# Kernel tuning notes

Measured on AMD Instinct MI355X. Metric: run time of the kernel, lower is better.

## Reference

```python
import jax, jax.numpy as jnp
import numpy as np

NUM_RELATIONS = 2
NUM_NODES = 100000


def rgcn_conv(x, edge_index, edge_type, weight, root, bias):
    """PyG RGCNConv with default aggr='mean':
    out[i] = bias + x[i] @ root + sum_r mean_{j in N_r(i)} (x[j] @ W_r)
    x: [N, Cin], edge_index: [2, E], weight: [R, Cin, Cout], root: [Cin, Cout]."""
    src, dst = edge_index[0], edge_index[1]
    x_src = x[src]                      # [E, Cin] gather
    out = x @ root + bias               # [N, Cout]
    for r in range(NUM_RELATIONS):      # small fixed loop over relations
        mask = (edge_type == r).astype(x.dtype)          # [E]
        msg = (x_src @ weight[r]) * mask[:, None]        # [E, Cout]
        agg = jax.ops.segment_sum(msg, dst, num_segments=NUM_NODES)
        deg = jax.ops.segment_sum(mask, dst, num_segments=NUM_NODES)
        out = out + agg / jnp.maximum(deg, 1.0)[:, None]
    return out


def setup_inputs() -> dict:
    key = jax.random.key(0)
    ks = jax.random.split(key, 16)
    Cin, Chid, Cout = 128, 256, 128
    E = 400000
    inp = {
        "x0": jax.random.normal(ks[0], (50000, 128), jnp.float32),
        "x1": jax.random.normal(ks[1], (50000, 64), jnp.float32),
        "edge_index": jax.random.randint(ks[2], (2, E), 0, NUM_NODES),
        "edge_type": jax.random.randint(ks[3], (E,), 0, NUM_RELATIONS),
        "dec_index": jax.random.randint(ks[4], (2, 100000), 0, NUM_NODES),
        # per-node-type input projections (Linear as x @ W + b)
        "lin0_w": jax.random.normal(ks[5], (128, Cin), jnp.float32) * 0.05,
        "lin0_b": jnp.zeros((Cin,), jnp.float32),
        "lin1_w": jax.random.normal(ks[6], (64, Cin), jnp.float32) * 0.05,
        "lin1_b": jnp.zeros((Cin,), jnp.float32),
        # RGCN layer 1
        "conv1_w": jax.random.normal(ks[7], (NUM_RELATIONS, Cin, Chid), jnp.float32) * 0.05,
        "conv1_root": jax.random.normal(ks[8], (Cin, Chid), jnp.float32) * 0.05,
        "conv1_b": jnp.zeros((Chid,), jnp.float32),
        # RGCN layer 2
        "conv2_w": jax.random.normal(ks[9], (NUM_RELATIONS, Chid, Cout), jnp.float32) * 0.05,
        "conv2_root": jax.random.normal(ks[10], (Chid, Cout), jnp.float32) * 0.05,
        "conv2_b": jnp.zeros((Cout,), jnp.float32),
        # decode head: Linear(2*Cout -> 1) + sigmoid
        "fc_w": jax.random.normal(ks[11], (2 * Cout, 1), jnp.float32) * 0.05,
        "fc_b": jnp.zeros((1,), jnp.float32),
    }
    return inp


def reference(x0, x1, edge_index, edge_type, dec_index,
              lin0_w, lin0_b, lin1_w, lin1_b,
              conv1_w, conv1_root, conv1_b,
              conv2_w, conv2_root, conv2_b,
              fc_w, fc_b):
    # trans_dimensions: per-type projection then concat along nodes
    x = jnp.concatenate([x0 @ lin0_w + lin0_b, x1 @ lin1_w + lin1_b], axis=0)  # [N, Cin]
    # encode (eval mode: dropout is identity)
    x = rgcn_conv(x, edge_index, edge_type, conv1_w, conv1_root, conv1_b)
    x = jax.nn.relu(x)
    z = rgcn_conv(x, edge_index, edge_type, conv2_w, conv2_root, conv2_b)
    # decode
    pair = jnp.concatenate([z[dec_index[0]], z[dec_index[1]]], axis=-1)  # [P, 2*Cout]
    return jax.nn.sigmoid(pair @ fc_w + fc_b)
```

## Files before the change

kernel.cpp:

```cpp
#include <hip/hip_runtime.h>
#include <hip/hip_bf16.h>
#include <math.h>

#define N_NODES 100000
#define N_EDGES 400000
#define N_PAIRS 100000
#define NBINS   200000

typedef short short8_t __attribute__((ext_vector_type(8)));
typedef float f32x4    __attribute__((ext_vector_type(4)));

__device__ __forceinline__ ushort f2bf(float f) {
    uint u = __float_as_uint(f);
    u += 0x7fffu + ((u >> 16) & 1u);
    return (ushort)(u >> 16);
}
__device__ __forceinline__ float bf2f(ushort b) {
    return __uint_as_float(((uint)b) << 16);
}
__device__ __forceinline__ uint packbf(float a, float b) {
    return (uint)f2bf(a) | ((uint)f2bf(b) << 16);
}

#define GLDS16(gp, lp) \
    __builtin_amdgcn_global_load_lds((const __attribute__((address_space(1))) uint*)(gp), \
                                     (__attribute__((address_space(3))) uint*)(lp), 16, 0, 0)

__global__ void cast_kernel(const float* __restrict__ in, ushort* __restrict__ outp, int n4) {
    int i = blockIdx.x * 256 + threadIdx.x;
    int stride = gridDim.x * 256;
    for (; i < n4; i += stride) {
        float4 v = ((const float4*)in)[i];
        ushort4 o;
        o.x = f2bf(v.x); o.y = f2bf(v.y); o.z = f2bf(v.z); o.w = f2bf(v.w);
        ((ushort4*)outp)[i] = o;
    }
}

__global__ void wlin_kernel(const float* __restrict__ w, ushort* __restrict__ wt, int K) {
    int i = blockIdx.x * 256 + threadIdx.x;
    if (i >= 128 * K) return;
    int n = i / K, k = i - n * K;
    wt[i] = f2bf(w[(size_t)k * 128 + n]);
}
__global__ void wc1_kernel(const float* __restrict__ root, const float* __restrict__ w,
                           ushort* __restrict__ wt) {
    int i = blockIdx.x * 256 + threadIdx.x;
    if (i >= 256 * 384) return;
    int n = i / 384, k = i % 384;
    float v;
    if (k < 128) v = root[(size_t)k * 256 + n];
    else         v = w[(size_t)(k - 128) * 256 + n];
    wt[(size_t)n * 384 + k] = f2bf(v);
}
__global__ void wc2_kernel(const float* __restrict__ root, const float* __restrict__ w,
                           ushort* __restrict__ wt) {
    int i = blockIdx.x * 256 + threadIdx.x;
    if (i >= 384 * 256) return;
    int n = i / 256, k = i % 256;
    float v;
    if (n < 128) v = root[(size_t)k * 128 + n];
    else         v = w[((size_t)((n >> 7) - 1) * 256 + k) * 128 + (n & 127)];
    wt[(size_t)n * 256 + k] = f2bf(v);
}

__global__ void hist_kernel(const int* __restrict__ dst, const int* __restrict__ et,
                            int* __restrict__ cnt) {
    int e = blockIdx.x * 256 + threadIdx.x;
    if (e < N_EDGES) atomicAdd(&cnt[et[e] * N_NODES + dst[e]], 1);
}

__global__ __launch_bounds__(1024) void scan1_kernel(const int* __restrict__ cnt,
                                                     int* __restrict__ ptr,
                                                     int* __restrict__ aux) {
    __shared__ int s[1024];
    int i = blockIdx.x * 1024 + threadIdx.x;
    int v = (i < NBINS) ? cnt[i] : 0;
    s[threadIdx.x] = v;
    __syncthreads();
    for (int off = 1; off < 1024; off <<= 1) {
        int t = (threadIdx.x >= off) ? s[threadIdx.x - off] : 0;
        __syncthreads();
        s[threadIdx.x] += t;
        __syncthreads();
    }
    if (i < NBINS) ptr[i] = s[threadIdx.x] - v;
    if (threadIdx.x == 1023) aux[blockIdx.x] = s[1023];
}

__global__ void scan2_kernel(int* __restrict__ aux, int nblk) {
    __shared__ int s[256];
    int v = (threadIdx.x < nblk) ? aux[threadIdx.x] : 0;
    s[threadIdx.x] = v;
    __syncthreads();
    for (int off = 1; off < 256; off <<= 1) {
        int t = (threadIdx.x >= off) ? s[threadIdx.x - off] : 0;
        __syncthreads();
        s[threadIdx.x] += t;
        __syncthreads();
    }
    if (threadIdx.x < nblk) aux[threadIdx.x] = s[threadIdx.x] - v;
}

__global__ void scan3_kernel(const int* __restrict__ aux, int* __restrict__ ptr,
                             int* __restrict__ cursor) {
    int i = blockIdx.x * 256 + threadIdx.x;
    if (i < NBINS) {
        int val = ptr[i] + aux[i >> 10];
        ptr[i] = val;
        cursor[i] = val;
    }
    if (i == 0) ptr[NBINS] = N_EDGES;
}

__global__ void fill_kernel(const int* __restrict__ src, const int* __restrict__ dst,
                            const int* __restrict__ et, int* __restrict__ cursor,
                            int* __restrict__ esorted) {
    int e = blockIdx.x * 256 + threadIdx.x;
    if (e < N_EDGES) {
        int b = et[e] * N_NODES + dst[e];
        int pos = atomicAdd(&cursor[b], 1);
        esorted[pos] = src[e];
    }
}

__global__ void gather1_kernel(const int* __restrict__ ptr, const int* __restrict__ es,
                               ushort* __restrict__ A1) {
    int d = blockIdx.x * 4 + (threadIdx.x >> 6);
    if (d >= N_NODES) return;
    int lane = threadIdx.x & 63;
    int p0 = ptr[d],           p1 = ptr[d + 1];
    int q0 = ptr[N_NODES + d], q1 = ptr[N_NODES + d + 1];
    int n0 = p1 - p0, n1 = q1 - q0;
    int n  = n0 > n1 ? n0 : n1;
    float a0 = 0, a1 = 0, b0 = 0, b1 = 0;
    for (int k = 0; k < n; k += 2) {
        uint v00 = 0, v01 = 0, v10 = 0, v11 = 0;
        if (k < n0)     v00 = *(const uint*)(A1 + (size_t)es[p0 + k] * 384 + lane * 2);
        if (k + 1 < n0) v01 = *(const uint*)(A1 + (size_t)es[p0 + k + 1] * 384 + lane * 2);
        if (k < n1)     v10 = *(const uint*)(A1 + (size_t)es[q0 + k] * 384 + lane * 2);
        if (k + 1 < n1) v11 = *(const uint*)(A1 + (size_t)es[q0 + k + 1] * 384 + lane * 2);
        a0 += bf2f((ushort)(v00 & 0xffffu)) + bf2f((ushort)(v01 & 0xffffu));
        a1 += bf2f((ushort)(v00 >> 16))     + bf2f((ushort)(v01 >> 16));
        b0 += bf2f((ushort)(v10 & 0xffffu)) + bf2f((ushort)(v11 & 0xffffu));
        b1 += bf2f((ushort)(v10 >> 16))     + bf2f((ushort)(v11 >> 16));
    }
    float i0 = n0 ? 1.0f / (float)n0 : 0.0f;
    float i1 = n1 ? 1.0f / (float)n1 : 0.0f;
    uint* row = (uint*)(A1 + (size_t)d * 384);
    row[64  + lane] = packbf(a0 * i0, a1 * i0);
    row[128 + lane] = packbf(b0 * i1, b1 * i1);
}

__global__ void combine2_kernel(const int* __restrict__ ptr, const int* __restrict__ es,
                                const ushort* __restrict__ H, ushort* __restrict__ zb) {
    int d = blockIdx.x * 4 + (threadIdx.x >> 6);
    if (d >= N_NODES) return;
    int lane = threadIdx.x & 63;
    int p0 = ptr[d],           p1 = ptr[d + 1];
    int q0 = ptr[N_NODES + d], q1 = ptr[N_NODES + d + 1];
    int n0 = p1 - p0, n1 = q1 - q0;
    int n  = n0 > n1 ? n0 : n1;
    uint rv = *(const uint*)(H + (size_t)d * 384 + lane * 2);
    float r0 = bf2f((ushort)(rv & 0xffffu)), r1 = bf2f((ushort)(rv >> 16));
    float a0 = 0, a1 = 0, b0 = 0, b1 = 0;
    for (int k = 0; k < n; k += 2) {
        uint v00 = 0, v01 = 0, v10 = 0, v11 = 0;
        if (k < n0)     v00 = *(const uint*)(H + (size_t)es[p0 + k] * 384 + 128 + lane * 2);
        if (k + 1 < n0) v01 = *(const uint*)(H + (size_t)es[p0 + k + 1] * 384 + 128 + lane * 2);
        if (k < n1)     v10 = *(const uint*)(H + (size_t)es[q0 + k] * 384 + 256 + lane * 2);
        if (k + 1 < n1) v11 = *(const uint*)(H + (size_t)es[q0 + k + 1] * 384 + 256 + lane * 2);
        a0 += bf2f((ushort)(v00 & 0xffffu)) + bf2f((ushort)(v01 & 0xffffu));
        a1 += bf2f((ushort)(v00 >> 16))     + bf2f((ushort)(v01 >> 16));
        b0 += bf2f((ushort)(v10 & 0xffffu)) + bf2f((ushort)(v11 & 0xffffu));
        b1 += bf2f((ushort)(v10 >> 16))     + bf2f((ushort)(v11 >> 16));
    }
    float i0 = n0 ? 1.0f / (float)n0 : 0.0f;
    float i1 = n1 ? 1.0f / (float)n1 : 0.0f;
    uint* orow = (uint*)(zb + (size_t)d * 128);
    orow[lane] = packbf(r0 + a0 * i0 + b0 * i1, r1 + a1 * i0 + b1 * i1);
}

template<int KTOT, int OST, int BIASN, bool RELU>
__global__ __launch_bounds__(256)
void mfma_gemm_kernel(const ushort* __restrict__ A, const ushort* __restrict__ Wt,
                      const float* __restrict__ bias, ushort* __restrict__ outp,
                      int nrows) {
    __shared__ short As[2][128 * 32];
    __shared__ short Bs[2][128 * 32];
    const int t  = threadIdx.x;
    const int m0 = blockIdx.x * 128;
    const int n0 = blockIdx.y * 128;
    const int lane = t & 63, w = t >> 6;
    const int wr = w >> 1, wc = w & 1;
    const int l15 = lane & 15, l4 = lane >> 4;

    const int row0 = t >> 2, off0 = (t & 3) * 8;
    int rg0 = m0 + row0;      if (rg0 >= nrows) rg0 = nrows - 1;
    int rg1 = m0 + row0 + 64; if (rg1 >= nrows) rg1 = nrows - 1;
    const ushort* a0p = A + (size_t)rg0 * KTOT + off0;
    const ushort* a1p = A + (size_t)rg1 * KTOT + off0;
    const ushort* b0p = Wt + (size_t)(n0 + row0) * KTOT + off0;
    const ushort* b1p = Wt + (size_t)(n0 + row0 + 64) * KTOT + off0;

#define STAGE(b, kg) do { \
        GLDS16(a0p + (kg), &As[b][t * 8]); \
        GLDS16(a1p + (kg), &As[b][(t + 256) * 8]); \
        GLDS16(b0p + (kg), &Bs[b][t * 8]); \
        GLDS16(b1p + (kg), &Bs[b][(t + 256) * 8]); \
    } while (0)

    f32x4 acc[4][4];
#pragma unroll
    for (int j = 0; j < 4; j++) {
        int col = n0 + wc * 64 + j * 16 + l15;
        float bv = (col < BIASN) ? bias[col] : 0.0f;
        f32x4 tmp = {bv, bv, bv, bv};
#pragma unroll
        for (int i = 0; i < 4; i++) acc[i][j] = tmp;
    }

    STAGE(0, 0);
    constexpr int NSTEP = KTOT / 32;
    for (int ks = 0; ks < NSTEP; ks++) {
        const int b = ks & 1;
        if (ks + 1 < NSTEP) {
            STAGE(b ^ 1, (ks + 1) * 32);
            asm volatile("s_waitcnt vmcnt(4)" ::: "memory");
        } else {
            asm volatile("s_waitcnt vmcnt(0)" ::: "memory");
        }
        asm volatile("s_barrier" ::: "memory");
        short8_t af[4], bfr[4];
#pragma unroll
        for (int i = 0; i < 4; i++)
            af[i] = *(short8_t*)&As[b][(wr * 64 + i * 16 + l15) * 32 + l4 * 8];
#pragma unroll
        for (int j = 0; j < 4; j++)
            bfr[j] = *(short8_t*)&Bs[b][(wc * 64 + j * 16 + l15) * 32 + l4 * 8];
#pragma unroll
        for (int i = 0; i < 4; i++)
#pragma unroll
            for (int j = 0; j < 4; j++)
                acc[i][j] = __builtin_amdgcn_mfma_f32_16x16x32_bf16(af[i], bfr[j], acc[i][j], 0, 0, 0);
        asm volatile("s_barrier" ::: "memory");
    }
#undef STAGE

#pragma unroll
    for (int i = 0; i < 4; i++) {
#pragma unroll
        for (int r = 0; r < 4; r++) {
            int row = m0 + wr * 64 + i * 16 + l4 * 4 + r;
            if (row < nrows) {
#pragma unroll
                for (int j = 0; j < 4; j++) {
                    int col = n0 + wc * 64 + j * 16 + l15;
                    float v = acc[i][j][r];
                    if (RELU) v = fmaxf(v, 0.0f);
                    outp[(size_t)row * OST + col] = f2bf(v);
                }
            }
        }
    }
}

__global__ void decode_kernel(const ushort* __restrict__ zb, const int* __restrict__ dec,
                              const float* __restrict__ fcw, const float* __restrict__ fcb,
                              float* __restrict__ out) {
    int wid  = blockIdx.x * 4 + (threadIdx.x >> 6);
    int lane = threadIdx.x & 63;
    if (wid >= N_PAIRS) return;
    int s = dec[wid];
    int d = dec[N_PAIRS + wid];
    uint vs = ((const uint*)(zb + (size_t)s * 128))[lane];
    uint vd = ((const uint*)(zb + (size_t)d * 128))[lane];
    float v = bf2f((ushort)(vs & 0xffffu)) * fcw[2 * lane]
            + bf2f((ushort)(vs >> 16))     * fcw[2 * lane + 1]
            + bf2f((ushort)(vd & 0xffffu)) * fcw[128 + 2 * lane]
            + bf2f((ushort)(vd >> 16))     * fcw[128 + 2 * lane + 1];
#pragma unroll
    for (int off = 32; off > 0; off >>= 1) v += __shfl_down(v, off);
    if (lane == 0) out[wid] = 1.0f / (1.0f + expf(-(v + fcb[0])));
}

extern "C" void kernel_launch(void* const* d_in, const int* in_sizes, int n_in,
                              void* d_out, int out_size, void* d_ws, size_t ws_size,
                              hipStream_t stream) {
    const float* x0        = (const float*)d_in[0];
    const float* x1        = (const float*)d_in[1];
    const int*   edge_idx  = (const int*)  d_in[2];
    const int*   edge_type = (const int*)  d_in[3];
    const int*   dec_index = (const int*)  d_in[4];
    const float* lin0_w    = (const float*)d_in[5];
    const float* lin0_b    = (const float*)d_in[6];
    const float* lin1_w    = (const float*)d_in[7];
    const float* lin1_b    = (const float*)d_in[8];
    const float* conv1_w   = (const float*)d_in[9];
    const float* conv1_root= (const float*)d_in[10];
    const float* conv1_b   = (const float*)d_in[11];
    const float* conv2_w   = (const float*)d_in[12];
    const float* conv2_root= (const float*)d_in[13];
    const float* conv2_b   = (const float*)d_in[14];
    const float* fc_w      = (const float*)d_in[15];
    const float* fc_b      = (const float*)d_in[16];
    float* out = (float*)d_out;

    char* W = (char*)d_ws;
    ushort* A1    = (ushort*)(W + 0);
    ushort* H     = (ushort*)(W + 0);
    ushort* y1    = (ushort*)(W + 76800000);
    ushort* zb    = (ushort*)(W + 76800000);
    int*    cnt   = (int*)   (W + 128000000);
    int*    ptrb  = (int*)   (W + 128800000);
    int*    cursor= (int*)   (W + 129600016);
    int*    aux   = (int*)   (W + 130400016);
    int*    esort = (int*)   (W + 130404112);
    ushort* wc1   = (ushort*)(W + 132004112);
    ushort* wc2   = (ushort*)(W + 132200720);
    ushort* wl0   = (ushort*)(W + 132397328);
    ushort* wl1   = (ushort*)(W + 132430096);
    ushort* x0bf  = (ushort*)(W + 132446480);
    ushort* x1bf  = (ushort*)(W + 145246480);

    const int* esrc = edge_idx;
    const int* edst = edge_idx + N_EDGES;

    hipMemsetAsync(cnt, 0, (size_t)NBINS * sizeof(int), stream);

    cast_kernel<<<2048, 256, 0, stream>>>(x0, x0bf, 50000 * 128 / 4);
    cast_kernel<<<2048, 256, 0, stream>>>(x1, x1bf, 50000 * 64 / 4);
    wlin_kernel<<<64, 256, 0, stream>>>(lin0_w, wl0, 128);
    wlin_kernel<<<32, 256, 0, stream>>>(lin1_w, wl1, 64);
    wc1_kernel<<<(256 * 384 + 255) / 256, 256, 0, stream>>>(conv1_root, conv1_w, wc1);
    wc2_kernel<<<(384 * 256 + 255) / 256, 256, 0, stream>>>(conv2_root, conv2_w, wc2);

    hist_kernel<<<(N_EDGES + 255) / 256, 256, 0, stream>>>(edst, edge_type, cnt);
    scan1_kernel<<<(NBINS + 1023) / 1024, 1024, 0, stream>>>(cnt, ptrb, aux);
    scan2_kernel<<<1, 256, 0, stream>>>(aux, (NBINS + 1023) / 1024);
    scan3_kernel<<<(NBINS + 255) / 256, 256, 0, stream>>>(aux, ptrb, cursor);
    fill_kernel<<<(N_EDGES + 255) / 256, 256, 0, stream>>>(esrc, edst, edge_type,
                                                           cursor, esort);

    mfma_gemm_kernel<128, 384, 128, false>
        <<<dim3(391, 1), 256, 0, stream>>>(x0bf, wl0, lin0_b, A1, 50000);
    mfma_gemm_kernel<64, 384, 128, false>
        <<<dim3(391, 1), 256, 0, stream>>>(x1bf, wl1, lin1_b,
                                           A1 + (size_t)50000 * 384, 50000);

    gather1_kernel<<<(N_NODES + 3) / 4, 256, 0, stream>>>(ptrb, esort, A1);
    mfma_gemm_kernel<384, 256, 256, true>
        <<<dim3(782, 2), 256, 0, stream>>>(A1, wc1, conv1_b, y1, N_NODES);

    mfma_gemm_kernel<256, 384, 128, false>
        <<<dim3(782, 3), 256, 0, stream>>>(y1, wc2, conv2_b, H, N_NODES);
    combine2_kernel<<<(N_NODES + 3) / 4, 256, 0, stream>>>(ptrb, esort, H, zb);

    decode_kernel<<<(N_PAIRS + 3) / 4, 256, 0, stream>>>(zb, dec_index, fc_w, fc_b, out);
}
```

Before: 282.8 us.

## Widen GEMM tiles to full N, triple-buffer LDS, and swizzle LDS layout

The MFMA GEMM now computes the full output width (128/256/384 columns) per block with 512 threads, instead of 128x128 tiles across a 2D grid. This lets each A row tile be loaded once rather than re-read per column block. It also moves from double to triple buffering with a two-stage-ahead prefetch, and XOR-swizzles the LDS chunk layout to reduce bank conflicts on fragment reads. In exchange, LDS use per block and register pressure are higher (up to FC=6 accumulator columns), which may lower occupancy.

```diff
diff --git a/kernel.cpp b/kernel.cpp
--- a/kernel.cpp
+++ b/kernel.cpp
@@ -25,6 +25,15 @@
 #define GLDS16(gp, lp) \
     __builtin_amdgcn_global_load_lds((const __attribute__((address_space(1))) uint*)(gp), \
                                      (__attribute__((address_space(3))) uint*)(lp), 16, 0, 0)
+
+template<int N> __device__ __forceinline__ void waitvm() {
+    if constexpr (N == 0)      asm volatile("s_waitcnt vmcnt(0)" ::: "memory");
+    else if constexpr (N == 2) asm volatile("s_waitcnt vmcnt(2)" ::: "memory");
+    else if constexpr (N == 3) asm volatile("s_waitcnt vmcnt(3)" ::: "memory");
+    else if constexpr (N == 4) asm volatile("s_waitcnt vmcnt(4)" ::: "memory");
+    else if constexpr (N == 6) asm volatile("s_waitcnt vmcnt(6)" ::: "memory");
+    else if constexpr (N == 8) asm volatile("s_waitcnt vmcnt(8)" ::: "memory");
+}
 
 __global__ void cast_kernel(const float* __restrict__ in, ushort* __restrict__ outp, int n4) {
     int i = blockIdx.x * 256 + threadIdx.x;
@@ -181,67 +190,78 @@
     orow[lane] = packbf(r0 + a0 * i0 + b0 * i1, r1 + a1 * i0 + b1 * i1);
 }
 
-template<int KTOT, int OST, int BIASN, bool RELU>
-__global__ __launch_bounds__(256)
+template<int KTOT, int BN, int OST, int BIASN, bool RELU>
+__global__ __launch_bounds__(512)
 void mfma_gemm_kernel(const ushort* __restrict__ A, const ushort* __restrict__ Wt,
                       const float* __restrict__ bias, ushort* __restrict__ outp,
                       int nrows) {
-    __shared__ short As[2][128 * 32];
-    __shared__ short Bs[2][128 * 32];
+    constexpr int FC = BN / 64;
+    constexpr int LB = BN / 128;
+    constexpr int L  = 1 + LB;
+    __shared__ short As[3][128 * 32];
+    __shared__ short Bs[3][BN * 32];
     const int t  = threadIdx.x;
     const int m0 = blockIdx.x * 128;
-    const int n0 = blockIdx.y * 128;
     const int lane = t & 63, w = t >> 6;
-    const int wr = w >> 1, wc = w & 1;
+    const int wr = w >> 2, wcl = w & 3;
     const int l15 = lane & 15, l4 = lane >> 4;
 
-    const int row0 = t >> 2, off0 = (t & 3) * 8;
-    int rg0 = m0 + row0;      if (rg0 >= nrows) rg0 = nrows - 1;
-    int rg1 = m0 + row0 + 64; if (rg1 >= nrows) rg1 = nrows - 1;
-    const ushort* a0p = A + (size_t)rg0 * KTOT + off0;
-    const ushort* a1p = A + (size_t)rg1 * KTOT + off0;
-    const ushort* b0p = Wt + (size_t)(n0 + row0) * KTOT + off0;
-    const ushort* b1p = Wt + (size_t)(n0 + row0 + 64) * KTOT + off0;
-
-#define STAGE(b, kg) do { \
-        GLDS16(a0p + (kg), &As[b][t * 8]); \
-        GLDS16(a1p + (kg), &As[b][(t + 256) * 8]); \
-        GLDS16(b0p + (kg), &Bs[b][t * 8]); \
-        GLDS16(b1p + (kg), &Bs[b][(t + 256) * 8]); \
+    const int arow = t >> 2;
+    const int sw_a = (((t & 3) ^ ((arow >> 1) & 3))) * 8;
+    int rg = m0 + arow; if (rg >= nrows) rg = nrows - 1;
+    const ushort* ap = A + (size_t)rg * KTOT + sw_a;
+    const ushort* bp[LB];
+#pragma unroll
+    for (int i = 0; i < LB; i++) {
+        int ch = t + i * 512;
+        int brow = ch >> 2;
+        bp[i] = Wt + (size_t)brow * KTOT + (((ch & 3) ^ ((brow >> 1) & 3))) * 8;
+    }
+
+#define STAGE(slot, kg) do { \
+        GLDS16(ap + (kg), &As[slot][t * 8]); \
+        _Pragma("unroll") \
+        for (int i_ = 0; i_ < LB; i_++) \
+            GLDS16(bp[i_] + (kg), &Bs[slot][(t + i_ * 512) * 8]); \
     } while (0)
 
-    f32x4 acc[4][4];
-#pragma unroll
-    for (int j = 0; j < 4; j++) {
-        int col = n0 + wc * 64 + j * 16 + l15;
+    f32x4 acc[4][FC];
+#pragma unroll
+    for (int j = 0; j < FC; j++) {
+        int col = wcl * (FC * 16) + j * 16 + l15;
         float bv = (col < BIASN) ? bias[col] : 0.0f;
         f32x4 tmp = {bv, bv, bv, bv};
 #pragma unroll
         for (int i = 0; i < 4; i++) acc[i][j] = tmp;
     }
 
+    const int xr = (l4 ^ ((l15 >> 1) & 3)) * 8;
+
     STAGE(0, 0);
+    STAGE(1, 32);
     constexpr int NSTEP = KTOT / 32;
     for (int ks = 0; ks < NSTEP; ks++) {
-        const int b = ks & 1;
-        if (ks + 1 < NSTEP) {
-            STAGE(b ^ 1, (ks + 1) * 32);
-            asm volatile("s_waitcnt vmcnt(4)" ::: "memory");
+        const int slot = ks % 3;
+        if (ks + 2 < NSTEP) {
+            STAGE((ks + 2) % 3, (ks + 2) * 32);
+            waitvm<2 * L>();
+        } else if (ks + 1 < NSTEP) {
+            waitvm<L>();
         } else {
-            asm volatile("s_waitcnt vmcnt(0)" ::: "memory");
+            waitvm<0>();
         }
         asm volatile("s_barrier" ::: "memory");
-        short8_t af[4], bfr[4];
+        short8_t af[4], bfr[FC];
 #pragma unroll
         for (int i = 0; i < 4; i++)
-            af[i] = *(short8_t*)&As[b][(wr * 64 + i * 16 + l15) * 32 + l4 * 8];
-#pragma unroll
-        for (int j = 0; j < 4; j++)
-            bfr[j] = *(short8_t*)&Bs[b][(wc * 64 + j * 16 + l15) * 32 + l4 * 8];
+            af[i] = *(short8_t*)&As[slot][(wr * 64 + i * 16 + l15) * 32 + xr];
+#pragma unroll
+        for (int j = 0; j < FC; j++)
+            bfr[j] = *(short8_t*)&Bs[slot][(wcl * (FC * 16) + j * 16 + l15) * 32 + xr];
 #pragma unroll
         for (int i = 0; i < 4; i++)
 #pragma unroll
-            for (int j = 0; j < 4; j++)
+            for (int j = 0; j < FC; j++)
                 acc[i][j] = __builtin_amdgcn_mfma_f32_16x16x32_bf16(af[i], bfr[j], acc[i][j], 0, 0, 0);
         asm volatile("s_barrier" ::: "memory");
     }
@@ -254,8 +274,8 @@
             int row = m0 + wr * 64 + i * 16 + l4 * 4 + r;
             if (row < nrows) {
 #pragma unroll
-                for (int j = 0; j < 4; j++) {
-                    int col = n0 + wc * 64 + j * 16 + l15;
+                for (int j = 0; j < FC; j++) {
+                    int col = wcl * (FC * 16) + j * 16 + l15;
                     float v = acc[i][j][r];
                     if (RELU) v = fmaxf(v, 0.0f);
                     outp[(size_t)row * OST + col] = f2bf(v);
@@ -342,18 +362,18 @@
     fill_kernel<<<(N_EDGES + 255) / 256, 256, 0, stream>>>(esrc, edst, edge_type,
                                                            cursor, esort);
 
-    mfma_gemm_kernel<128, 384, 128, false>
-        <<<dim3(391, 1), 256, 0, stream>>>(x0bf, wl0, lin0_b, A1, 50000);
-    mfma_gemm_kernel<64, 384, 128, false>
-        <<<dim3(391, 1), 256, 0, stream>>>(x1bf, wl1, lin1_b,
-                                           A1 + (size_t)50000 * 384, 50000);
+    mfma_gemm_kernel<128, 128, 384, 128, false>
+        <<<391, 512, 0, stream>>>(x0bf, wl0, lin0_b, A1, 50000);
+    mfma_gemm_kernel<64, 128, 384, 128, false>
+        <<<391, 512, 0, stream>>>(x1bf, wl1, lin1_b,
+                                  A1 + (size_t)50000 * 384, 50000);
 
     gather1_kernel<<<(N_NODES + 3) / 4, 256, 0, stream>>>(ptrb, esort, A1);
-    mfma_gemm_kernel<384, 256, 256, true>
-        <<<dim3(782, 2), 256, 0, stream>>>(A1, wc1, conv1_b, y1, N_NODES);
-
-    mfma_gemm_kernel<256, 384, 128, false>
-        <<<dim3(782, 3), 256, 0, stream>>>(y1, wc2, conv2_b, H, N_NODES);
+    mfma_gemm_kernel<384, 256, 256, 256, true>
+        <<<782, 512, 0, stream>>>(A1, wc1, conv1_b, y1, N_NODES);
+
+    mfma_gemm_kernel<256, 384, 384, 128, false>
+        <<<782, 512, 0, stream>>>(y1, wc2, conv2_b, H, N_NODES);
     combine2_kernel<<<(N_NODES + 3) / 4, 256, 0, stream>>>(ptrb, esort, H, zb);
 
     decode_kernel<<<(N_PAIRS + 3) / 4, 256, 0, stream>>>(zb, dec_index, fc_w, fc_b, out);
```

Result: no change. 287.3 us (+1.6%).

## Triple-buffer GEMM loads, swizzle LDS layout, and remap blocks across XCDs

Applied to the files above, without the earlier changes.

The MFMA GEMM moves from double to triple buffering of LDS tiles, so two k-steps of global-to-LDS loads are in flight while the current one is consumed. The k-chunk columns in LDS are XOR-swizzled by row to cut bank conflicts on the short8 fragment reads. The 2D grid becomes a 1D grid whose block index is remapped so that consecutive work tiles land on the same XCD, which should improve L2 reuse of the shared weight tiles. In exchange, LDS use rises by half and occupancy may drop.

```diff
diff --git a/kernel.cpp b/kernel.cpp
--- a/kernel.cpp
+++ b/kernel.cpp
@@ -25,6 +25,12 @@
 #define GLDS16(gp, lp) \
     __builtin_amdgcn_global_load_lds((const __attribute__((address_space(1))) uint*)(gp), \
                                      (__attribute__((address_space(3))) uint*)(lp), 16, 0, 0)
+
+template<int N> __device__ __forceinline__ void waitvm() {
+    if constexpr (N == 0)      asm volatile("s_waitcnt vmcnt(0)" ::: "memory");
+    else if constexpr (N == 4) asm volatile("s_waitcnt vmcnt(4)" ::: "memory");
+    else if constexpr (N == 8) asm volatile("s_waitcnt vmcnt(8)" ::: "memory");
+}
 
 __global__ void cast_kernel(const float* __restrict__ in, ushort* __restrict__ outp, int n4) {
     int i = blockIdx.x * 256 + threadIdx.x;
@@ -181,33 +187,41 @@
     orow[lane] = packbf(r0 + a0 * i0 + b0 * i1, r1 + a1 * i0 + b1 * i1);
 }
 
-template<int KTOT, int OST, int BIASN, bool RELU>
+template<int KTOT, int NP, int OST, int BIASN, bool RELU>
 __global__ __launch_bounds__(256)
 void mfma_gemm_kernel(const ushort* __restrict__ A, const ushort* __restrict__ Wt,
                       const float* __restrict__ bias, ushort* __restrict__ outp,
-                      int nrows) {
-    __shared__ short As[2][128 * 32];
-    __shared__ short Bs[2][128 * 32];
-    const int t  = threadIdx.x;
-    const int m0 = blockIdx.x * 128;
-    const int n0 = blockIdx.y * 128;
+                      int nrows, int mtiles) {
+    __shared__ short As[3][128 * 32];
+    __shared__ short Bs[3][128 * 32];
+    const int t = threadIdx.x;
     const int lane = t & 63, w = t >> 6;
     const int wr = w >> 1, wc = w & 1;
     const int l15 = lane & 15, l4 = lane >> 4;
 
-    const int row0 = t >> 2, off0 = (t & 3) * 8;
-    int rg0 = m0 + row0;      if (rg0 >= nrows) rg0 = nrows - 1;
-    int rg1 = m0 + row0 + 64; if (rg1 >= nrows) rg1 = nrows - 1;
-    const ushort* a0p = A + (size_t)rg0 * KTOT + off0;
-    const ushort* a1p = A + (size_t)rg1 * KTOT + off0;
-    const ushort* b0p = Wt + (size_t)(n0 + row0) * KTOT + off0;
-    const ushort* b1p = Wt + (size_t)(n0 + row0 + 64) * KTOT + off0;
-
-#define STAGE(b, kg) do { \
-        GLDS16(a0p + (kg), &As[b][t * 8]); \
-        GLDS16(a1p + (kg), &As[b][(t + 256) * 8]); \
-        GLDS16(b0p + (kg), &Bs[b][t * 8]); \
-        GLDS16(b1p + (kg), &Bs[b][(t + 256) * 8]); \
+    const int nwg = mtiles * NP;
+    const int q = nwg >> 3, r = nwg & 7;
+    const int orig = blockIdx.x;
+    const int xcd = orig & 7;
+    const int work = (xcd < r ? xcd * (q + 1) : r * (q + 1) + (xcd - r) * q) + (orig >> 3);
+    const int mt = work / NP;
+    const int m0 = mt * 128;
+    const int n0 = (work - mt * NP) * 128;
+
+    const int arow = t >> 2;
+    const int swc = ((t & 3) ^ ((arow >> 1) & 3)) * 8;
+    int rg0 = m0 + arow;      if (rg0 >= nrows) rg0 = nrows - 1;
+    int rg1 = m0 + arow + 64; if (rg1 >= nrows) rg1 = nrows - 1;
+    const ushort* ap0 = A + (size_t)rg0 * KTOT + swc;
+    const ushort* ap1 = A + (size_t)rg1 * KTOT + swc;
+    const ushort* bp0 = Wt + (size_t)(n0 + arow) * KTOT + swc;
+    const ushort* bp1 = Wt + (size_t)(n0 + arow + 64) * KTOT + swc;
+
+#define STAGE(slot, kg) do { \
+        GLDS16(ap0 + (kg), &As[slot][t * 8]); \
+        GLDS16(ap1 + (kg), &As[slot][(t + 256) * 8]); \
+        GLDS16(bp0 + (kg), &Bs[slot][t * 8]); \
+        GLDS16(bp1 + (kg), &Bs[slot][(t + 256) * 8]); \
     } while (0)
 
     f32x4 acc[4][4];
@@ -220,24 +234,29 @@
         for (int i = 0; i < 4; i++) acc[i][j] = tmp;
     }
 
+    const int xr = (l4 ^ ((l15 >> 1) & 3)) * 8;
+
+    constexpr int NSTEP = KTOT / 32;
     STAGE(0, 0);
-    constexpr int NSTEP = KTOT / 32;
+    if (NSTEP > 1) STAGE(1, 32);
     for (int ks = 0; ks < NSTEP; ks++) {
-        const int b = ks & 1;
-        if (ks + 1 < NSTEP) {
-            STAGE(b ^ 1, (ks + 1) * 32);
-            asm volatile("s_waitcnt vmcnt(4)" ::: "memory");
+        const int slot = ks % 3;
+        if (ks + 2 < NSTEP) {
+            STAGE((ks + 2) % 3, (ks + 2) * 32);
+            waitvm<8>();
+        } else if (ks + 1 < NSTEP) {
+            waitvm<4>();
         } else {
-            asm volatile("s_waitcnt vmcnt(0)" ::: "memory");
+            waitvm<0>();
         }
         asm volatile("s_barrier" ::: "memory");
         short8_t af[4], bfr[4];
 #pragma unroll
         for (int i = 0; i < 4; i++)
-            af[i] = *(short8_t*)&As[b][(wr * 64 + i * 16 + l15) * 32 + l4 * 8];
+            af[i] = *(short8_t*)&As[slot][(wr * 64 + i * 16 + l15) * 32 + xr];
 #pragma unroll
         for (int j = 0; j < 4; j++)
-            bfr[j] = *(short8_t*)&Bs[b][(wc * 64 + j * 16 + l15) * 32 + l4 * 8];
+            bfr[j] = *(short8_t*)&Bs[slot][(wc * 64 + j * 16 + l15) * 32 + xr];
 #pragma unroll
         for (int i = 0; i < 4; i++)
 #pragma unroll
@@ -250,13 +269,13 @@
 #pragma unroll
     for (int i = 0; i < 4; i++) {
 #pragma unroll
-        for (int r = 0; r < 4; r++) {
-            int row = m0 + wr * 64 + i * 16 + l4 * 4 + r;
+        for (int r2 = 0; r2 < 4; r2++) {
+            int row = m0 + wr * 64 + i * 16 + l4 * 4 + r2;
             if (row < nrows) {
 #pragma unroll
                 for (int j = 0; j < 4; j++) {
                     int col = n0 + wc * 64 + j * 16 + l15;
-                    float v = acc[i][j][r];
+                    float v = acc[i][j][r2];
                     if (RELU) v = fmaxf(v, 0.0f);
                     outp[(size_t)row * OST + col] = f2bf(v);
                 }
@@ -342,18 +361,18 @@
     fill_kernel<<<(N_EDGES + 255) / 256, 256, 0, stream>>>(esrc, edst, edge_type,
                                                            cursor, esort);
 
-    mfma_gemm_kernel<128, 384, 128, false>
-        <<<dim3(391, 1), 256, 0, stream>>>(x0bf, wl0, lin0_b, A1, 50000);
-    mfma_gemm_kernel<64, 384, 128, false>
-        <<<dim3(391, 1), 256, 0, stream>>>(x1bf, wl1, lin1_b,
-                                           A1 + (size_t)50000 * 384, 50000);
+    mfma_gemm_kernel<128, 1, 384, 128, false>
+        <<<391, 256, 0, stream>>>(x0bf, wl0, lin0_b, A1, 50000, 391);
+    mfma_gemm_kernel<64, 1, 384, 128, false>
+        <<<391, 256, 0, stream>>>(x1bf, wl1, lin1_b,
+                                  A1 + (size_t)50000 * 384, 50000, 391);
 
     gather1_kernel<<<(N_NODES + 3) / 4, 256, 0, stream>>>(ptrb, esort, A1);
-    mfma_gemm_kernel<384, 256, 256, true>
-        <<<dim3(782, 2), 256, 0, stream>>>(A1, wc1, conv1_b, y1, N_NODES);
-
-    mfma_gemm_kernel<256, 384, 128, false>
-        <<<dim3(782, 3), 256, 0, stream>>>(y1, wc2, conv2_b, H, N_NODES);
+    mfma_gemm_kernel<384, 2, 256, 256, true>
+        <<<1564, 256, 0, stream>>>(A1, wc1, conv1_b, y1, N_NODES, 782);
+
+    mfma_gemm_kernel<256, 3, 384, 128, false>
+        <<<2346, 256, 0, stream>>>(y1, wc2, conv2_b, H, N_NODES, 782);
     combine2_kernel<<<(N_NODES + 3) / 4, 256, 0, stream>>>(ptrb, esort, H, zb);
 
     decode_kernel<<<(N_PAIRS + 3) / 4, 256, 0, stream>>>(zb, dec_index, fc_w, fc_b, out);
```

New measurement: 274.3 us. 3.0% less time.
